# Kernel tuning notes

Measured on AMD Instinct MI355X. Metric: run time of the kernel, lower is better.

The kernel has to match this reference:

```python
import jax, jax.numpy as jnp
import numpy as np

GENETIC_CODE = {'TTT': 'F', 'TTC': 'F', 'TTA': 'L', 'TTG': 'L', 'CTT': 'L', 'CTC': 'L', 'CTA': 'L', 'CTG': 'L', 'ATT': 'I', 'ATC': 'I', 'ATA': 'I', 'ATG': 'M', 'GTT': 'V', 'GTC': 'V', 'GTA': 'V', 'GTG': 'V', 'TCT': 'S', 'TCC': 'S', 'TCA': 'S', 'TCG': 'S', 'AGT': 'S', 'AGC': 'S', 'CCT': 'P', 'CCC': 'P', 'CCA': 'P', 'CCG': 'P', 'ACT': 'T', 'ACC': 'T', 'ACA': 'T', 'ACG': 'T', 'GCT': 'A', 'GCC': 'A', 'GCA': 'A', 'GCG': 'A', 'TAT': 'Y', 'TAC': 'Y', 'TAA': '*', 'TAG': '*', 'TGA': '*', 'CAT': 'H', 'CAC': 'H', 'CAA': 'Q', 'CAG': 'Q', 'AAT': 'N', 'AAC': 'N', 'AAA': 'K', 'AAG': 'K', 'GAT': 'D', 'GAC': 'D', 'GAA': 'E', 'GAG': 'E', 'TGT': 'C', 'TGC': 'C', 'TGG': 'W', 'CGT': 'R', 'CGC': 'R', 'CGA': 'R', 'CGG': 'R', 'AGA': 'R', 'AGG': 'R', 'GGT': 'G', 'GGC': 'G', 'GGA': 'G', 'GGG': 'G'}
NUC_TO_IDX = {'T': 0, 'C': 1, 'A': 2, 'G': 3}

def _build_syn_bias(synonymy_bias=1.0):
    idx = lambda c: NUC_TO_IDX[c[0]] * 16 + NUC_TO_IDX[c[1]] * 4 + NUC_TO_IDX[c[2]]
    groups = {}
    for codon, aa in GENETIC_CODE.items():
        groups.setdefault(aa, []).append(idx(codon))
    m = np.zeros((64, 64), dtype=np.float32)
    for codons in groups.values():
        for i in codons:
            for j in codons:
                m[i, j] = synonymy_bias
    return jnp.asarray(m)

HIDDEN, N_HEADS = 256, 4
HEAD_DIM = HIDDEN // N_HEADS
B, S = 2, 4096

def setup_inputs() -> dict:
    key = jax.random.key(0)
    ks = jax.random.split(key, 10)
    std = 1.0 / np.sqrt(HIDDEN)
    lin = lambda k: jax.random.uniform(k, (HIDDEN, HIDDEN), jnp.float32, -std, std)
    bias = lambda k: jax.random.uniform(k, (HIDDEN,), jnp.float32, -std, std)
    return {
        'x': jax.random.normal(ks[0], (B, S, HIDDEN), jnp.float32),
        'codons': jax.random.randint(ks[1], (B, S), 0, 64),
        'syn_bias': _build_syn_bias(1.0),
        'wq': lin(ks[2]), 'bq': bias(ks[3]),
        'wk': lin(ks[4]), 'bk': bias(ks[5]),
        'wv': lin(ks[6]), 'bv': bias(ks[7]),
        'wo': lin(ks[8]), 'bo': bias(ks[9]),
    }

def reference(x, codons, syn_bias, wq, bq, wk, bk, wv, bv, wo, bo):
    b, s, _ = x.shape
    split = lambda t: t.reshape(b, s, N_HEADS, HEAD_DIM).transpose(0, 2, 1, 3)  # (B,H,S,D)
    q = split(x @ wq.T + bq)
    k = split(x @ wk.T + bk)
    v = split(x @ wv.T + bv)
    scores = jnp.einsum('bhqd,bhkd->bhqk', q, k) / np.sqrt(HEAD_DIM)
    # gather pairwise synonymy bias: (B,S,S) broadcast over heads
    pair_bias = syn_bias[codons[:, :, None], codons[:, None, :]]
    scores = scores + pair_bias[:, None, :, :]
    attn = jax.nn.softmax(scores, axis=-1)
    out = jnp.einsum('bhqk,bhkd->bhqd', attn, v)
    out = out.transpose(0, 2, 1, 3).reshape(b, s, HIDDEN)
    return out @ wo.T + bo
```

## Files before the change

### kernel.cpp

```cpp
#include <hip/hip_runtime.h>
#include <hip/hip_bf16.h>

#define NH 4
#define HD 64
#define HID 256
#define SS 4096

#define QFRAG_PER_HEAD (128 * 6 * 64 * 8)
#define KFRAG_PER_HEAD (64 * 12 * 64 * 8)
#define VFRAG_PER_HEAD (64 * 8 * 64 * 8)

typedef float f4 __attribute__((ext_vector_type(4)));
typedef float f16v __attribute__((ext_vector_type(16)));
typedef short bf8 __attribute__((ext_vector_type(8)));
typedef unsigned int u4v __attribute__((ext_vector_type(4)));

static __device__ __forceinline__ float fast_exp2(float x) {
#if __has_builtin(__builtin_amdgcn_exp2f)
    return __builtin_amdgcn_exp2f(x);
#else
    float r; asm("v_exp_f32 %0, %1" : "=v"(r) : "v"(x)); return r;
#endif
}

static __device__ __forceinline__ unsigned pack2(float a, float b) {
    unsigned ua = (unsigned)__bfloat16_as_ushort(__float2bfloat16(a));
    unsigned ub = (unsigned)__bfloat16_as_ushort(__float2bfloat16(b));
    return ua | (ub << 16);
}

static __device__ __forceinline__ unsigned cvtpk(float a, float b) {
    unsigned r;
    asm("v_cvt_pk_bf16_f32 %0, %1, %2" : "=v"(r) : "v"(a), "v"(b));
    return r;
}

__global__ void setup_kernel(const float* __restrict__ syn,
                             int* __restrict__ gid, float* __restrict__ betaP)
{
    const int lane = threadIdx.x;
    int rep = 64;
    for (int j = 63; j >= 0; --j)
        if (syn[lane * 64 + j] != 0.0f) rep = j;
    if (rep == 64) rep = lane;
    unsigned long long m = __ballot(rep == lane);
    int id = (int)__popcll(m & ((2ull << rep) - 1ull)) - 1;
    if (id < 0) id = 0;
    gid[lane] = id;
    if (lane == 0) *betaP = syn[0] * 1.44269504088896f;
}

__global__ __launch_bounds__(256)
void pack_w_kernel(const float* __restrict__ wq, const float* __restrict__ wk,
                   const float* __restrict__ wv, const float* __restrict__ wo,
                   __hip_bfloat16* __restrict__ wpk)
{
    const int t = blockIdx.x * 256 + threadIdx.x;
    const int mat = t >> 13;
    const int r = t & 8191;
    const int dt = r >> 10, ks = (r >> 6) & 15, lane = r & 63;
    const float* w = (mat == 0) ? wq : (mat == 1) ? wk : (mat == 2) ? wv : wo;
    const int row = dt * 32 + (lane & 31);
    const int col = ks * 16 + (lane >> 5) * 8;
    const f4 a = *(const f4*)&w[(size_t)row * 256 + col];
    const f4 b = *(const f4*)&w[(size_t)row * 256 + col + 4];
    union { unsigned u[4]; bf8 v; } o;
    o.u[0] = pack2(a[0], a[1]); o.u[1] = pack2(a[2], a[3]);
    o.u[2] = pack2(b[0], b[1]); o.u[3] = pack2(b[2], b[3]);
    *(bf8*)&wpk[(size_t)t * 8] = o.v;
}

__global__ __launch_bounds__(256)
void qkv_mfma_kernel(const float* __restrict__ x,
                     const __hip_bfloat16* __restrict__ wpk,
                     const float* __restrict__ bq, const float* __restrict__ bk,
                     const float* __restrict__ bv,
                     const int* __restrict__ codons,
                     const int* __restrict__ gid, const float* __restrict__ betaP,
                     __hip_bfloat16* __restrict__ qfrag,
                     __hip_bfloat16* __restrict__ kfrag,
                     __hip_bfloat16* __restrict__ vfrag)
{
    const int bid = blockIdx.x;
    const int stile = bid / 6;
    const int grp = bid % 6;
    const int tid = threadIdx.x;
    const int w = tid >> 6, lane = tid & 63, hi = lane >> 5, l5 = lane & 31;

    const int bidx = stile >> 7;
    const int stl = stile & 127;
    const int hs = stl & 1, tkv = stl >> 1;

    __shared__ __hip_bfloat16 xs[32][256];

    {
        const int r0 = tid >> 5, c = tid & 31;
        #pragma unroll
        for (int it = 0; it < 4; ++it) {
            const int row = r0 + it * 8;
            const f4 a = *(const f4*)&x[(size_t)(stile * 32 + row) * HID + c * 8];
            const f4 b2 = *(const f4*)&x[(size_t)(stile * 32 + row) * HID + c * 8 + 4];
            union { unsigned u[4]; bf8 v; } o;
            o.u[0] = pack2(a[0], a[1]); o.u[1] = pack2(a[2], a[3]);
            o.u[2] = pack2(b2[0], b2[1]); o.u[3] = pack2(b2[2], b2[3]);
            *(bf8*)&xs[row][((c ^ row) & 31) * 8] = o.v;
        }
    }
    __syncthreads();

    const int t24 = grp * 4 + w;
    const int mat = t24 >> 3;
    const int dt = t24 & 7;
    const int head = dt >> 1, d32 = dt & 1;

    const __hip_bfloat16* wb = wpk + (size_t)((mat * 8 + dt) * 16) * 512 + (size_t)lane * 8;
    bf8 wf[16];
    #pragma unroll
    for (int ks = 0; ks < 16; ++ks) wf[ks] = *(const bf8*)&wb[ks * 512];

    f16v acc;
    #pragma unroll
    for (int r = 0; r < 16; ++r) acc[r] = 0.0f;

    if (mat < 2) {
        #pragma unroll
        for (int ks = 0; ks < 16; ++ks) {
            const bf8 xf = *(const bf8*)&xs[l5][(((ks * 2 + hi) ^ l5) & 31) * 8];
            acc = __builtin_amdgcn_mfma_f32_32x32x16_bf16(wf[ks], xf, acc, 0, 0, 0);
        }
    } else {
        #pragma unroll
        for (int ks = 0; ks < 16; ++ks) {
            const bf8 xf = *(const bf8*)&xs[l5][(((ks * 2 + hi) ^ l5) & 31) * 8];
            acc = __builtin_amdgcn_mfma_f32_32x32x16_bf16(xf, wf[ks], acc, 0, 0, 0);
        }
    }

    const float QSCALE = 0.18033688011112042f;
    if (mat == 0) {
        f4 b4[4];
        #pragma unroll
        for (int j = 0; j < 4; ++j)
            b4[j] = *(const f4*)&bq[head * 64 + d32 * 32 + j * 8 + 4 * hi];
        #pragma unroll
        for (int r = 0; r < 16; ++r) acc[r] = (acc[r] + b4[r >> 2][r & 3]) * QSCALE;
    } else if (mat == 1) {
        f4 b4[4];
        #pragma unroll
        for (int j = 0; j < 4; ++j)
            b4[j] = *(const f4*)&bk[head * 64 + d32 * 32 + j * 8 + 4 * hi];
        #pragma unroll
        for (int r = 0; r < 16; ++r) acc[r] += b4[r >> 2][r & 3];
    } else {
        const float bn = bv[head * 64 + d32 * 32 + l5];
        #pragma unroll
        for (int r = 0; r < 16; ++r) acc[r] += bn;
    }

    unsigned wd[8];
    #pragma unroll
    for (int i = 0; i < 8; ++i) wd[i] = pack2(acc[2 * i], acc[2 * i + 1]);
    const unsigned e0 = (unsigned)__shfl_xor((int)(hi ? wd[0] : wd[2]), 32, 64);
    const unsigned e1 = (unsigned)__shfl_xor((int)(hi ? wd[1] : wd[3]), 32, 64);
    const unsigned e2 = (unsigned)__shfl_xor((int)(hi ? wd[4] : wd[6]), 32, 64);
    const unsigned e3 = (unsigned)__shfl_xor((int)(hi ? wd[5] : wd[7]), 32, 64);
    union { unsigned u[4]; bf8 v; } fa, fb;
    if (hi == 0) {
        fa.u[0] = wd[0]; fa.u[1] = wd[1]; fa.u[2] = e0; fa.u[3] = e1;
        fb.u[0] = wd[4]; fb.u[1] = wd[5]; fb.u[2] = e2; fb.u[3] = e3;
    } else {
        fa.u[0] = e0; fa.u[1] = e1; fa.u[2] = wd[2]; fa.u[3] = wd[3];
        fb.u[0] = e2; fb.u[1] = e3; fb.u[2] = wd[6]; fb.u[3] = wd[7];
    }

    const int hd = bidx * NH + head;
    if (mat == 0) {
        __hip_bfloat16* qb = qfrag + (size_t)hd * QFRAG_PER_HEAD;
        *(bf8*)&qb[((size_t)(stl * 6 + d32 * 2 + 0) * 64 + lane) * 8] = fa.v;
        *(bf8*)&qb[((size_t)(stl * 6 + d32 * 2 + 1) * 64 + lane) * 8] = fb.v;
    } else if (mat == 1) {
        __hip_bfloat16* kb = kfrag + (size_t)hd * KFRAG_PER_HEAD;
        *(bf8*)&kb[((size_t)(tkv * 12 + d32 * 4 + hs) * 64 + lane) * 8] = fa.v;
        *(bf8*)&kb[((size_t)(tkv * 12 + d32 * 4 + 2 + hs) * 64 + lane) * 8] = fb.v;
    } else {
        __hip_bfloat16* vb = vfrag + (size_t)hd * VFRAG_PER_HEAD;
        const int ja = ((stl * 2 + 0) & 3) * 2 + d32;
        const int jb = ((stl * 2 + 1) & 3) * 2 + d32;
        *(bf8*)&vb[((size_t)(tkv * 8 + ja) * 64 + lane) * 8] = fa.v;
        *(bf8*)&vb[((size_t)(tkv * 8 + jb) * 64 + lane) * 8] = fb.v;
    }

    if (grp == 0) {
        const int hh = w;
        const int hd2 = bidx * NH + hh;
        __hip_bfloat16* qb = qfrag + (size_t)hd2 * QFRAG_PER_HEAD;
        __hip_bfloat16* kb = kfrag + (size_t)hd2 * KFRAG_PER_HEAD;
        u4v z; z[0] = 0; z[1] = 0; z[2] = 0; z[3] = 0;
        *(u4v*)&qb[((size_t)(stl * 6 + 4) * 64 + lane) * 8] = z;
        *(u4v*)&qb[((size_t)(stl * 6 + 5) * 64 + lane) * 8] = z;
        *(u4v*)&kb[((size_t)(tkv * 12 + 8 + hs) * 64 + lane) * 8] = z;
        *(u4v*)&kb[((size_t)(tkv * 12 + 10 + hs) * 64 + lane) * 8] = z;
        asm volatile("s_waitcnt vmcnt(0)" ::: "memory");
        if (hi == 0) {
            const int cg = gid[codons[bidx * SS + stl * 32 + l5] & 63];
            const float bl2e = *betaP;
            const int lt = ((cg >> 3) & 1) * 32 + l5;
            qb[((size_t)(stl * 6 + 4 + (cg >> 4)) * 64 + lt) * 8 + (cg & 7)] =
                __float2bfloat16(bl2e);
            kb[((size_t)(tkv * 12 + 8 + (cg >> 4) * 2 + hs) * 64 + lt) * 8 + (cg & 7)] =
                __float2bfloat16(1.0f);
        }
    }
}

__global__ __launch_bounds__(256, 4)
void attn_kernel(const __hip_bfloat16* __restrict__ qfrag,
                 const __hip_bfloat16* __restrict__ kfrag,
                 const __hip_bfloat16* __restrict__ vfrag,
                 __hip_bfloat16* __restrict__ po0,
                 __hip_bfloat16* __restrict__ po1,
                 __hip_bfloat16* __restrict__ po2,
                 __hip_bfloat16* __restrict__ po3,
                 float* __restrict__ ls0, float* __restrict__ ls1,
                 float* __restrict__ ls2, float* __restrict__ ls3)
{
    const int bid = blockIdx.x;
    const int bh = bid & 7;
    const int b = bh >> 2, h = bh & 3;
    const int quarter = (bid >> 3) & 3;
    const int qg = bid >> 5;
    const int tid = threadIdx.x;
    const int w = tid >> 6;
    const int lane = tid & 63;
    const int q5 = lane & 31;
    const int hi = lane >> 5;

    __shared__ __align__(16) char smem[40960];

    const char* kT = (const char*)(kfrag + (size_t)(b * NH + h) * KFRAG_PER_HEAD);
    const char* vT = (const char*)(vfrag + (size_t)(b * NH + h) * VFRAG_PER_HEAD);

    const int stl = qg * 4 + w;
    const __hip_bfloat16* qb = qfrag + (size_t)(b * NH + h) * QFRAG_PER_HEAD
                               + ((size_t)stl * 6 * 64 + lane) * 8;
    bf8 qf[6];
    #pragma unroll
    for (int ks = 0; ks < 6; ++ks) qf[ks] = *(const bf8*)&qb[ks * 512];

    f16v oacc0, oacc1;
    #pragma unroll
    for (int r = 0; r < 16; ++r) { oacc0[r] = 0.0f; oacc1[r] = 0.0f; }
    float lrun = 0.0f;

    const int w5 = w * 5;
    const int tt0 = quarter * 16;

    auto stage = [&](int buf, int t) {
        const int tt = tt0 + t;
        #pragma unroll
        for (int c = 0; c < 5; ++c) {
            const int id = w5 + c;
            const char* src = (id < 12)
                ? kT + (size_t)tt * 12288 + (size_t)id * 1024
                : vT + (size_t)tt * 8192 + (size_t)(id - 12) * 1024;
            __builtin_amdgcn_global_load_lds(
                (const __attribute__((address_space(1))) unsigned int*)(src + lane * 16),
                (__attribute__((address_space(3))) unsigned int*)(smem + buf * 20480 + id * 1024),
                16, 0, 0);
        }
    };

    stage(0, 0);
    __syncthreads();

    int cur = 0;
    #pragma unroll 1
    for (int t = 0; t < 16; ++t) {
        if (t + 1 < 16) stage(cur ^ 1, t + 1);

        const char* kb = smem + cur * 20480 + lane * 16;

        f16v sA, sB;
        #pragma unroll
        for (int r = 0; r < 16; ++r) { sA[r] = 0.0f; sB[r] = 0.0f; }
        __builtin_amdgcn_s_setprio(1);
        #pragma unroll
        for (int ks = 0; ks < 6; ++ks) {
            const bf8 k0 = *(const bf8*)(kb + (2 * ks) * 1024);
            const bf8 k1 = *(const bf8*)(kb + (2 * ks + 1) * 1024);
            sA = __builtin_amdgcn_mfma_f32_32x32x16_bf16(k0, qf[ks], sA, 0, 0, 0);
            sB = __builtin_amdgcn_mfma_f32_32x32x16_bf16(k1, qf[ks], sB, 0, 0, 0);
        }
        __builtin_amdgcn_s_setprio(0);

        float ls = 0.0f;
        #pragma unroll
        for (int r = 0; r < 16; ++r) { sA[r] = fast_exp2(sA[r]); ls += sA[r]; }
        #pragma unroll
        for (int r = 0; r < 16; ++r) { sB[r] = fast_exp2(sB[r]); ls += sB[r]; }
        lrun += ls;

        unsigned dwv[2][4][2];
        #pragma unroll
        for (int j = 0; j < 4; ++j)
            #pragma unroll
            for (int c = 0; c < 2; ++c) {
                dwv[0][j][c] = cvtpk(sA[j * 4 + 2 * c], sA[j * 4 + 2 * c + 1]);
                dwv[1][j][c] = cvtpk(sB[j * 4 + 2 * c], sB[j * 4 + 2 * c + 1]);
            }
        unsigned rc[2][2][2];
        #pragma unroll
        for (int t2 = 0; t2 < 2; ++t2)
            #pragma unroll
            for (int k1 = 0; k1 < 2; ++k1)
                #pragma unroll
                for (int c = 0; c < 2; ++c) {
                    const unsigned snd = hi ? dwv[t2][2 * k1][c] : dwv[t2][2 * k1 + 1][c];
                    rc[t2][k1][c] = (unsigned)__shfl_xor((int)snd, 32, 64);
                }
        bf8 pfv[4];
        #pragma unroll
        for (int ks = 0; ks < 4; ++ks) {
            const int t2 = ks >> 1, k1 = ks & 1;
            union { unsigned u[4]; bf8 v; } pu;
            pu.u[0] = hi ? rc[t2][k1][0] : dwv[t2][2 * k1][0];
            pu.u[1] = hi ? rc[t2][k1][1] : dwv[t2][2 * k1][1];
            pu.u[2] = hi ? dwv[t2][2 * k1 + 1][0] : rc[t2][k1][0];
            pu.u[3] = hi ? dwv[t2][2 * k1 + 1][1] : rc[t2][k1][1];
            pfv[ks] = pu.v;
        }

        __builtin_amdgcn_s_setprio(1);
        #pragma unroll
        for (int ks = 0; ks < 4; ++ks) {
            const bf8 v0 = *(const bf8*)(kb + (12 + 2 * ks) * 1024);
            const bf8 v1 = *(const bf8*)(kb + (13 + 2 * ks) * 1024);
            oacc0 = __builtin_amdgcn_mfma_f32_32x32x16_bf16(v0, pfv[ks], oacc0, 0, 0, 0);
            oacc1 = __builtin_amdgcn_mfma_f32_32x32x16_bf16(v1, pfv[ks], oacc1, 0, 0, 0);
        }
        __builtin_amdgcn_s_setprio(0);

        __syncthreads();
        cur ^= 1;
    }

    const float ltot = lrun + __shfl_xor(lrun, 32, 64);
    float* osh = (float*)smem;
    float* lsh = (float*)(smem + 33792);
    #pragma unroll
    for (int r = 0; r < 16; ++r) {
        const int d = (r & 3) + 8 * (r >> 2) + 4 * hi;
        osh[(w * 32 + q5) * 66 + d] = oacc0[r];
        osh[(w * 32 + q5) * 66 + 32 + d] = oacc1[r];
    }
    if (hi == 0) lsh[w * 32 + q5] = ltot;
    __syncthreads();

    __hip_bfloat16* pob = (quarter == 0) ? po0 : (quarter == 1) ? po1
                        : (quarter == 2) ? po2 : po3;
    float* lsb = (quarter == 0) ? ls0 : (quarter == 1) ? ls1
               : (quarter == 2) ? ls2 : ls3;
    const int row = tid >> 1;
    const int dh = (tid & 1) * 32;
    const float* src = &osh[row * 66 + dh];
    __hip_bfloat16* dst = pob + ((size_t)(b * SS + qg * 128 + row) * HID + h * HD + dh);
    #pragma unroll
    for (int j = 0; j < 4; ++j) {
        const f4 x0 = *(const f4*)&src[j * 8];
        const f4 x1 = *(const f4*)&src[j * 8 + 4];
        union { unsigned u[4]; bf8 v; } o;
        o.u[0] = pack2(x0[0], x0[1]); o.u[1] = pack2(x0[2], x0[3]);
        o.u[2] = pack2(x1[0], x1[1]); o.u[3] = pack2(x1[2], x1[3]);
        *(bf8*)&dst[j * 8] = o.v;
    }
    if (tid < 128) lsb[(size_t)(b * SS + qg * 128 + tid) * 4 + h] = lsh[tid];
}

__global__ __launch_bounds__(256)
void out_proj_kernel(const __hip_bfloat16* __restrict__ po0,
                     const __hip_bfloat16* __restrict__ po1,
                     const __hip_bfloat16* __restrict__ po2,
                     const __hip_bfloat16* __restrict__ po3,
                     const float* __restrict__ ls0, const float* __restrict__ ls1,
                     const float* __restrict__ ls2, const float* __restrict__ ls3,
                     const __hip_bfloat16* __restrict__ wpk,
                     const float* __restrict__ bo, float* __restrict__ out)
{
    const int bid = blockIdx.x;
    const int stile = bid >> 1, grp = bid & 1;
    const int tid = threadIdx.x;
    const int w = tid >> 6, lane = tid & 63, hi = lane >> 5, l5 = lane & 31;

    __shared__ __hip_bfloat16 xs[32][256];
    {
        const int r0 = tid >> 5, c = tid & 31;
        #pragma unroll
        for (int it = 0; it < 4; ++it) {
            const int row = r0 + it * 8;
            const size_t srow = (size_t)stile * 32 + row;
            const int head = c >> 3;
            const float inv = 1.0f / (ls0[srow * 4 + head] + ls1[srow * 4 + head]
                                    + ls2[srow * 4 + head] + ls3[srow * 4 + head]);
            union { bf8 v; unsigned u[4]; } a0, a1, a2, a3;
            a0.v = *(const bf8*)&po0[srow * 256 + c * 8];
            a1.v = *(const bf8*)&po1[srow * 256 + c * 8];
            a2.v = *(const bf8*)&po2[srow * 256 + c * 8];
            a3.v = *(const bf8*)&po3[srow * 256 + c * 8];
            union { unsigned u[4]; bf8 v; } o;
            #pragma unroll
            for (int i = 0; i < 4; ++i) {
                const float lo = __uint_as_float(a0.u[i] << 16)
                               + __uint_as_float(a1.u[i] << 16)
                               + __uint_as_float(a2.u[i] << 16)
                               + __uint_as_float(a3.u[i] << 16);
                const float hv = __uint_as_float(a0.u[i] & 0xffff0000u)
                               + __uint_as_float(a1.u[i] & 0xffff0000u)
                               + __uint_as_float(a2.u[i] & 0xffff0000u)
                               + __uint_as_float(a3.u[i] & 0xffff0000u);
                o.u[i] = pack2(lo * inv, hv * inv);
            }
            *(bf8*)&xs[row][((c ^ row) & 31) * 8] = o.v;
        }
    }
    __syncthreads();

    const int nt = grp * 4 + w;
    const __hip_bfloat16* wb = wpk + (size_t)((3 * 8 + nt) * 16) * 512 + (size_t)lane * 8;
    bf8 wf[16];
    #pragma unroll
    for (int ks = 0; ks < 16; ++ks) wf[ks] = *(const bf8*)&wb[ks * 512];

    f16v acc;
    #pragma unroll
    for (int r = 0; r < 16; ++r) acc[r] = 0.0f;
    #pragma unroll
    for (int ks = 0; ks < 16; ++ks) {
        const bf8 xf = *(const bf8*)&xs[l5][(((ks * 2 + hi) ^ l5) & 31) * 8];
        acc = __builtin_amdgcn_mfma_f32_32x32x16_bf16(xf, wf[ks], acc, 0, 0, 0);
    }

    const float bn = bo[nt * 32 + l5];
    #pragma unroll
    for (int r = 0; r < 16; ++r) {
        const int sloc = (r & 3) + 8 * (r >> 2) + 4 * hi;
        out[(size_t)(stile * 32 + sloc) * HID + nt * 32 + l5] = acc[r] + bn;
    }
}

extern "C" void kernel_launch(void* const* d_in, const int* in_sizes, int n_in,
                              void* d_out, int out_size, void* d_ws, size_t ws_size,
                              hipStream_t stream)
{
    (void)in_sizes; (void)n_in; (void)out_size; (void)ws_size;
    const float* x        = (const float*)d_in[0];
    const int*   codons   = (const int*)d_in[1];
    const float* syn_bias = (const float*)d_in[2];
    const float* wq = (const float*)d_in[3];
    const float* bq = (const float*)d_in[4];
    const float* wk = (const float*)d_in[5];
    const float* bk = (const float*)d_in[6];
    const float* wv = (const float*)d_in[7];
    const float* bv = (const float*)d_in[8];
    const float* wo = (const float*)d_in[9];
    const float* bo = (const float*)d_in[10];
    float* out = (float*)d_out;

    char* ws = (char*)d_ws;
    int*   gid   = (int*)(ws);
    float* betaP = (float*)(ws + 256);
    __hip_bfloat16* wpk   = (__hip_bfloat16*)(ws + 4096);
    __hip_bfloat16* qfrag = (__hip_bfloat16*)(ws + (size_t)1048576u);
    __hip_bfloat16* kfrag = (__hip_bfloat16*)(ws + (size_t)7340032u);
    __hip_bfloat16* vfrag = (__hip_bfloat16*)(ws + (size_t)13631488u);
    __hip_bfloat16* po0   = (__hip_bfloat16*)(ws + (size_t)17825792u);
    __hip_bfloat16* po1   = (__hip_bfloat16*)(ws + (size_t)22020096u);
    __hip_bfloat16* po2   = (__hip_bfloat16*)(ws + (size_t)26214400u);
    __hip_bfloat16* po3   = (__hip_bfloat16*)(ws + (size_t)30408704u);
    float* ls0            = (float*)(ws + (size_t)34603008u);
    float* ls1            = (float*)(ws + (size_t)34734080u);
    float* ls2            = (float*)(ws + (size_t)34865152u);
    float* ls3            = (float*)(ws + (size_t)34996224u);

    setup_kernel<<<1, 64, 0, stream>>>(syn_bias, gid, betaP);
    pack_w_kernel<<<128, 256, 0, stream>>>(wq, wk, wv, wo, wpk);
    qkv_mfma_kernel<<<1536, 256, 0, stream>>>(x, wpk, bq, bk, bv, codons, gid, betaP,
                                              qfrag, kfrag, vfrag);
    attn_kernel<<<1024, 256, 0, stream>>>(qfrag, kfrag, vfrag,
                                          po0, po1, po2, po3, ls0, ls1, ls2, ls3);
    out_proj_kernel<<<512, 256, 0, stream>>>(po0, po1, po2, po3,
                                             ls0, ls1, ls2, ls3, wpk, bo, out);
}
```

Baseline: 89.77 us.

## Fold setup into pack kernel, use permlane32 swap, drop setprio

Merges the tiny setup kernel into the weight-packing kernel, which removes one launch. In the attention inner loop, the cross-half exchange of P fragments now uses v_permlane32_swap instead of __shfl_xor plus selects, cutting LDS/bpermute traffic and VALU selects. It also removes the s_setprio hints around the MFMA blocks, which may change how waves interleave.

```diff
diff --git a/kernel.cpp b/kernel.cpp
--- a/kernel.cpp
+++ b/kernel.cpp
@@ -35,26 +35,26 @@
     return r;
 }
 
-__global__ void setup_kernel(const float* __restrict__ syn,
-                             int* __restrict__ gid, float* __restrict__ betaP)
-{
-    const int lane = threadIdx.x;
-    int rep = 64;
-    for (int j = 63; j >= 0; --j)
-        if (syn[lane * 64 + j] != 0.0f) rep = j;
-    if (rep == 64) rep = lane;
-    unsigned long long m = __ballot(rep == lane);
-    int id = (int)__popcll(m & ((2ull << rep) - 1ull)) - 1;
-    if (id < 0) id = 0;
-    gid[lane] = id;
-    if (lane == 0) *betaP = syn[0] * 1.44269504088896f;
-}
-
 __global__ __launch_bounds__(256)
 void pack_w_kernel(const float* __restrict__ wq, const float* __restrict__ wk,
                    const float* __restrict__ wv, const float* __restrict__ wo,
+                   const float* __restrict__ syn,
+                   int* __restrict__ gid, float* __restrict__ betaP,
                    __hip_bfloat16* __restrict__ wpk)
 {
+    if (blockIdx.x == 0 && threadIdx.x < 64) {
+        const int lane = threadIdx.x;
+        int rep = 64;
+        for (int j = 63; j >= 0; --j)
+            if (syn[lane * 64 + j] != 0.0f) rep = j;
+        if (rep == 64) rep = lane;
+        unsigned long long m = __ballot(rep == lane);
+        int id = (int)__popcll(m & ((2ull << rep) - 1ull)) - 1;
+        if (id < 0) id = 0;
+        gid[lane] = id;
+        if (lane == 0) *betaP = syn[0] * 1.44269504088896f;
+    }
+
     const int t = blockIdx.x * 256 + threadIdx.x;
     const int mat = t >> 13;
     const int r = t & 8191;
@@ -283,7 +283,6 @@
         f16v sA, sB;
         #pragma unroll
         for (int r = 0; r < 16; ++r) { sA[r] = 0.0f; sB[r] = 0.0f; }
-        __builtin_amdgcn_s_setprio(1);
         #pragma unroll
         for (int ks = 0; ks < 6; ++ks) {
             const bf8 k0 = *(const bf8*)(kb + (2 * ks) * 1024);
@@ -291,7 +290,6 @@
             sA = __builtin_amdgcn_mfma_f32_32x32x16_bf16(k0, qf[ks], sA, 0, 0, 0);
             sB = __builtin_amdgcn_mfma_f32_32x32x16_bf16(k1, qf[ks], sB, 0, 0, 0);
         }
-        __builtin_amdgcn_s_setprio(0);
 
         float ls = 0.0f;
         #pragma unroll
@@ -300,37 +298,32 @@
         for (int r = 0; r < 16; ++r) { sB[r] = fast_exp2(sB[r]); ls += sB[r]; }
         lrun += ls;
 
-        unsigned dwv[2][4][2];
-        #pragma unroll
-        for (int j = 0; j < 4; ++j)
+        bf8 pfv[4];
+        #pragma unroll
+        for (int t2 = 0; t2 < 2; ++t2) {
+            const f16v& s = t2 ? sB : sA;
+            unsigned dwv[4][2];
             #pragma unroll
-            for (int c = 0; c < 2; ++c) {
-                dwv[0][j][c] = cvtpk(sA[j * 4 + 2 * c], sA[j * 4 + 2 * c + 1]);
-                dwv[1][j][c] = cvtpk(sB[j * 4 + 2 * c], sB[j * 4 + 2 * c + 1]);
-            }
-        unsigned rc[2][2][2];
-        #pragma unroll
-        for (int t2 = 0; t2 < 2; ++t2)
+            for (int j = 0; j < 4; ++j)
+                #pragma unroll
+                for (int c = 0; c < 2; ++c)
+                    dwv[j][c] = cvtpk(s[j * 4 + 2 * c], s[j * 4 + 2 * c + 1]);
             #pragma unroll
-            for (int k1 = 0; k1 < 2; ++k1)
+            for (int k1 = 0; k1 < 2; ++k1) {
+                union { unsigned u[4]; bf8 v; } pu;
                 #pragma unroll
                 for (int c = 0; c < 2; ++c) {
-                    const unsigned snd = hi ? dwv[t2][2 * k1][c] : dwv[t2][2 * k1 + 1][c];
-                    rc[t2][k1][c] = (unsigned)__shfl_xor((int)snd, 32, 64);
+                    unsigned a = dwv[2 * k1][c];
+                    unsigned bch = dwv[2 * k1 + 1][c];
+                    asm volatile("v_permlane32_swap_b32 %0, %1"
+                                 : "+v"(a), "+v"(bch));
+                    pu.u[c] = a;
+                    pu.u[2 + c] = bch;
                 }
-        bf8 pfv[4];
-        #pragma unroll
-        for (int ks = 0; ks < 4; ++ks) {
-            const int t2 = ks >> 1, k1 = ks & 1;
-            union { unsigned u[4]; bf8 v; } pu;
-            pu.u[0] = hi ? rc[t2][k1][0] : dwv[t2][2 * k1][0];
-            pu.u[1] = hi ? rc[t2][k1][1] : dwv[t2][2 * k1][1];
-            pu.u[2] = hi ? dwv[t2][2 * k1 + 1][0] : rc[t2][k1][0];
-            pu.u[3] = hi ? dwv[t2][2 * k1 + 1][1] : rc[t2][k1][1];
-            pfv[ks] = pu.v;
-        }
-
-        __builtin_amdgcn_s_setprio(1);
+                pfv[t2 * 2 + k1] = pu.v;
+            }
+        }
+
         #pragma unroll
         for (int ks = 0; ks < 4; ++ks) {
             const bf8 v0 = *(const bf8*)(kb + (12 + 2 * ks) * 1024);
@@ -338,7 +331,6 @@
             oacc0 = __builtin_amdgcn_mfma_f32_32x32x16_bf16(v0, pfv[ks], oacc0, 0, 0, 0);
             oacc1 = __builtin_amdgcn_mfma_f32_32x32x16_bf16(v1, pfv[ks], oacc1, 0, 0, 0);
         }
-        __builtin_amdgcn_s_setprio(0);
 
         __syncthreads();
         cur ^= 1;
@@ -481,8 +473,7 @@
     float* ls2            = (float*)(ws + (size_t)34865152u);
     float* ls3            = (float*)(ws + (size_t)34996224u);
 
-    setup_kernel<<<1, 64, 0, stream>>>(syn_bias, gid, betaP);
-    pack_w_kernel<<<128, 256, 0, stream>>>(wq, wk, wv, wo, wpk);
+    pack_w_kernel<<<128, 256, 0, stream>>>(wq, wk, wv, wo, syn_bias, gid, betaP, wpk);
     qkv_mfma_kernel<<<1536, 256, 0, stream>>>(x, wpk, bq, bk, bv, codons, gid, betaP,
                                               qfrag, kfrag, vfrag);
     attn_kernel<<<1024, 256, 0, stream>>>(qfrag, kfrag, vfrag,
```

Result: faster. 84.74 us (-5.6%).
